# Optimization experiments

Hardware: AMD Instinct MI355X
Metric: run time of the kernel (lower is better)

The kernel has to match this reference:

```python
import jax, jax.numpy as jnp
import numpy as np

N = 100000   # nodes
E = 1600000  # edges
C = 128      # num_features == out_channels
L = 3        # num_layers


def setup_inputs() -> dict:
    key = jax.random.key(0)
    ks = jax.random.split(key, 7)
    x = jax.random.normal(ks[0], (N, C), dtype=jnp.float32)
    edge_index = jax.random.randint(ks[1], (2, E), 0, N, dtype=jnp.int64)
    # GatedGraphConv per-layer linear weights [L, C, C]
    weight = jax.random.normal(ks[2], (L, C, C), dtype=jnp.float32) / np.sqrt(C)
    # shared GRUCell params (torch layout: [3C, C] rows = r, z, n)
    w_ih = jax.random.normal(ks[3], (3 * C, C), dtype=jnp.float32) / np.sqrt(C)
    w_hh = jax.random.normal(ks[4], (3 * C, C), dtype=jnp.float32) / np.sqrt(C)
    b_ih = jax.random.normal(ks[5], (3 * C,), dtype=jnp.float32) * 0.01
    b_hh = jax.random.normal(ks[6], (3 * C,), dtype=jnp.float32) * 0.01
    return {"x": x, "edge_index": edge_index, "weight": weight,
            "w_ih": w_ih, "w_hh": w_hh, "b_ih": b_ih, "b_hh": b_hh}


def _gru_cell(inp, h, w_ih, w_hh, b_ih, b_hh):
    gi = inp @ w_ih.T + b_ih  # [N, 3C]
    gh = h @ w_hh.T + b_hh    # [N, 3C]
    i_r, i_z, i_n = jnp.split(gi, 3, axis=1)
    h_r, h_z, h_n = jnp.split(gh, 3, axis=1)
    r = jax.nn.sigmoid(i_r + h_r)
    z = jax.nn.sigmoid(i_z + h_z)
    n = jnp.tanh(i_n + r * h_n)
    return (1.0 - z) * n + z * h


def reference(x, edge_index, weight, w_ih, w_hh, b_ih, b_hh):
    src, dst = edge_index[0], edge_index[1]
    n_nodes = x.shape[0]
    # mean aggregation denominators (in-degree, 0-degree nodes -> 0 output)
    counts = jax.ops.segment_sum(jnp.ones(src.shape[0], dtype=x.dtype), dst,
                                 num_segments=n_nodes)
    denom = jnp.maximum(counts, 1.0)[:, None]
    h = x
    for i in range(weight.shape[0]):
        m = h @ weight[i]                                   # [N, C]
        agg = jax.ops.segment_sum(m[src], dst, num_segments=n_nodes) / denom
        h = _gru_cell(agg, h, w_ih, w_hh, b_ih, b_hh)
    # x.mean(1).unsqueeze(1) -> [N, 1], then tanh
    return jnp.tanh(jnp.mean(h, axis=1, keepdims=True))
```

## Files before the change

### kernel.cpp

```cpp
#include <hip/hip_runtime.h>
#include <math.h>

#define NN 100000
#define NE 1600000
#define CC 128
#define C3 384
#define SCAN_B 256
#define SCAN_NB ((NN + SCAN_B - 1) / SCAN_B)

typedef __attribute__((ext_vector_type(4))) float f4;
typedef __attribute__((ext_vector_type(8))) short s8;

__device__ __forceinline__ float sigmoidf_(float x) { return 1.0f / (1.0f + __expf(-x)); }
__device__ __forceinline__ float tanhf_(float x) { return 2.0f / (1.0f + __expf(-2.0f * x)) - 1.0f; }

__device__ __forceinline__ short f2bf(float x) {
    unsigned u = __float_as_uint(x);
    unsigned r = (u + 0x7fffu + ((u >> 16) & 1u)) >> 16;
    return (short)r;
}
__device__ __forceinline__ float bf2f(short s) {
    return __uint_as_float(((unsigned)(unsigned short)s) << 16);
}

__device__ __forceinline__ int detect_flag(const int* e32) {
    int allz = 1;
#pragma unroll
    for (int i = 0; i < 32; i++)
        if (e32[2 * i + 1] != 0) allz = 0;
    return allz;
}

__device__ __forceinline__ int edge_val(const void* edges, int f, long long idx) {
    return f ? (int)((const long long*)edges)[idx] : ((const int*)edges)[idx];
}

__global__ void k_count(const void* __restrict__ edges, int* __restrict__ counts) {
    __shared__ int sf;
    if (threadIdx.x == 0) sf = detect_flag((const int*)edges);
    __syncthreads();
    int f = sf;
    int e = blockIdx.x * blockDim.x + threadIdx.x;
    if (e < NE) {
        int d = edge_val(edges, f, (long long)NE + e);
        atomicAdd(&counts[d], 1);
    }
}

__global__ void k_scan1(const int* __restrict__ counts, int* __restrict__ bsum) {
    __shared__ int red[4];
    int t = threadIdx.x;
    int i = blockIdx.x * SCAN_B + t;
    int v = (i < NN) ? counts[i] : 0;
#pragma unroll
    for (int off = 32; off; off >>= 1) v += __shfl_down(v, off);
    if ((t & 63) == 0) red[t >> 6] = v;
    __syncthreads();
    if (t == 0) bsum[blockIdx.x] = red[0] + red[1] + red[2] + red[3];
}

__global__ void k_scan2(const int* __restrict__ bsum, int* __restrict__ boff,
                        int* __restrict__ coarse_cursor) {
    __shared__ int lds[512];
    int t = threadIdx.x;
    int v = (t < SCAN_NB) ? bsum[t] : 0;
    lds[t] = v;
    __syncthreads();
    for (int off = 1; off < 512; off <<= 1) {
        int u = (t >= off) ? lds[t - off] : 0;
        __syncthreads();
        lds[t] += u;
        __syncthreads();
    }
    if (t < SCAN_NB) {
        int ex = lds[t] - v;
        boff[t] = ex;
        coarse_cursor[t] = ex;
    }
}

__global__ void k_scan3(const int* __restrict__ counts, const int* __restrict__ boff,
                        int* __restrict__ rowptr, float* __restrict__ inv_denom) {
    __shared__ int lds[SCAN_B];
    int t = threadIdx.x;
    int i = blockIdx.x * SCAN_B + t;
    int v = (i < NN) ? counts[i] : 0;
    lds[t] = v;
    __syncthreads();
    for (int off = 1; off < SCAN_B; off <<= 1) {
        int u = (t >= off) ? lds[t - off] : 0;
        __syncthreads();
        lds[t] += u;
        __syncthreads();
    }
    if (i < NN) {
        rowptr[i] = boff[blockIdx.x] + lds[t] - v;
        inv_denom[i] = 1.0f / (float)((v > 1) ? v : 1);
    }
    if (i == 0) rowptr[NN] = NE;
}

__global__ __launch_bounds__(1024) void k_part(const void* __restrict__ edges,
                                               int* __restrict__ coarse_cursor,
                                               uint2* __restrict__ tmp) {
    __shared__ int hist[SCAN_NB];
    __shared__ int base[SCAN_NB];
    __shared__ int sf;
    int t = threadIdx.x;
    if (t == 0) sf = detect_flag((const int*)edges);
    long long e0 = (long long)blockIdx.x * 8192;

    for (int c = t; c < SCAN_NB; c += 1024) hist[c] = 0;
    __syncthreads();
    int f = sf;

    int src[8], dst[8];
#pragma unroll
    for (int i = 0; i < 8; i++) {
        long long e = e0 + i * 1024 + t;
        if (e < NE) {
            src[i] = edge_val(edges, f, e);
            dst[i] = edge_val(edges, f, NE + e);
            atomicAdd(&hist[dst[i] >> 8], 1);
        } else {
            dst[i] = -1;
        }
    }
    __syncthreads();
    for (int c = t; c < SCAN_NB; c += 1024) {
        int h = hist[c];
        base[c] = (h > 0) ? atomicAdd(&coarse_cursor[c], h) : 0;
        hist[c] = 0;
    }
    __syncthreads();
#pragma unroll
    for (int i = 0; i < 8; i++) {
        if (dst[i] >= 0) {
            int c = dst[i] >> 8;
            int off = atomicAdd(&hist[c], 1);
            tmp[base[c] + off] = make_uint2((unsigned)src[i], (unsigned)dst[i]);
        }
    }
}

__global__ void k_fine(const uint2* __restrict__ tmp, const int* __restrict__ rowptr,
                       int* __restrict__ csr_src) {
    __shared__ int cur[256];
    int c = blockIdx.x;
    int t = threadIdx.x;
    int d = c * 256 + t;
    cur[t] = (d <= NN) ? rowptr[d < NN ? d : NN] : NE;
    __syncthreads();
    int start = rowptr[c * 256];
    int endd = (c * 256 + 256 <= NN) ? rowptr[c * 256 + 256] : NE;
    for (int p = start + t; p < endd; p += 256) {
        uint2 pr = tmp[p];
        int slot = atomicAdd(&cur[pr.y & 255], 1);
        csr_src[slot] = (int)pr.x;
    }
}

__global__ void k_prep(const float* __restrict__ weight, const float* __restrict__ w_ih,
                       const float* __restrict__ w_hh, const float* __restrict__ b_ih,
                       const float* __restrict__ b_hh,
                       short* __restrict__ B1hi, short* __restrict__ B1lo,
                       short* __restrict__ B2hi, short* __restrict__ B2lo,
                       float* __restrict__ bvec) {
    const int P1 = 3 * C3 * CC;
    int gid = blockIdx.x * blockDim.x + threadIdx.x;
    if (gid < P1) {
        int i = gid / (C3 * CC);
        int rem = gid % (C3 * CC);
        int j = rem / CC;
        int k = rem % CC;
        const float* Wr = weight + i * CC * CC + k * CC;
        const float* ir = w_ih + j * CC;
        float v = 0.f;
#pragma unroll 4
        for (int c = 0; c < CC; c++) v += Wr[c] * ir[c];
        short hi = f2bf(v);
        short lo = f2bf(v - bf2f(hi));
        if (j < 256) {
            int idx = i * 65536 + j * 256 + k;
            B1hi[idx] = hi; B1lo[idx] = lo;
        } else {
            int idx = i * 32768 + (j - 256) * 128 + k;
            B2hi[idx] = hi; B2lo[idx] = lo;
        }
    } else if (gid < 2 * P1) {
        int g = gid - P1;
        int i = g / (C3 * CC);
        int rem = g % (C3 * CC);
        int j = rem / CC;
        int k = rem % CC;
        float v = w_hh[j * CC + k];
        short hi = f2bf(v);
        short lo = f2bf(v - bf2f(hi));
        if (j < 256) {
            int idx = i * 65536 + j * 256 + 128 + k;
            B1hi[idx] = hi; B1lo[idx] = lo;
        } else {
            int idx = i * 32768 + (j - 256 + 128) * 128 + k;
            B2hi[idx] = hi; B2lo[idx] = lo;
        }
    } else if (gid < 2 * P1 + 512) {
        int j = gid - 2 * P1;
        float v;
        if (j < 256) v = b_ih[j] + b_hh[j];
        else if (j < 384) v = b_ih[j];
        else v = b_hh[j - 128];
        bvec[j] = v;
    }
}

__global__ void k_cvt(const float* __restrict__ x, unsigned short* __restrict__ hhi,
                      unsigned short* __restrict__ hlo) {
    long long g = ((long long)blockIdx.x * 256 + threadIdx.x) * 8;
    float4 v0 = *(const float4*)(x + g);
    float4 v1 = *(const float4*)(x + g + 4);
    float f[8] = {v0.x, v0.y, v0.z, v0.w, v1.x, v1.y, v1.z, v1.w};
    s8 oh, ol;
#pragma unroll
    for (int q = 0; q < 8; q++) {
        short hi = f2bf(f[q]);
        oh[q] = hi;
        ol[q] = f2bf(f[q] - bf2f(hi));
    }
    *(s8*)(hhi + g) = oh;
    *(s8*)(hlo + g) = ol;
}

__global__ __launch_bounds__(512, 4) void k_fused(
    const unsigned short* __restrict__ hhi_i, const unsigned short* __restrict__ hlo_i,
    unsigned short* __restrict__ hhi_o, unsigned short* __restrict__ hlo_o,
    const int* __restrict__ rowptr, const int* __restrict__ csr_src,
    const float* __restrict__ inv_denom,
    const short* __restrict__ B1hi, const short* __restrict__ B1lo,
    const short* __restrict__ B2hi, const short* __restrict__ B2lo,
    const float* __restrict__ bvec) {
    __shared__ short Ahi[16384];
    __shared__ short Alo[16384];
    int t = threadIdx.x;
    long long nb = (long long)blockIdx.x * 64;
    int wv = t >> 6;
    int L = t & 63;

#pragma unroll
    for (int i = 0; i < 2; i++) {
        int ci = t + 512 * i;
        int rr = ci >> 4;
        int c = ci & 15;
        int c4 = 16 + c;
        long long row = nb + rr;
        if (row >= NN) row = NN - 1;
        int off = (c4 >> 2) * 2048 + (rr >> 4) * 512 + (rr & 15) * 32 + (c4 & 3) * 8;
        long long gsrc = row * CC + c * 8;
        *(s8*)&Ahi[off] = *(const s8*)(hhi_i + gsrc);
        *(s8*)&Alo[off] = *(const s8*)(hlo_i + gsrc);
    }

    {
        int q = L >> 4;
        int l16 = L & 15;
#pragma unroll
        for (int pass = 0; pass < 2; pass++) {
            int rr = wv * 8 + pass * 4 + q;
            long long rowc = nb + rr;
            if (rowc >= NN) rowc = NN - 1;
            int lo = rowptr[rowc], hi = rowptr[rowc + 1];
            float acc0[8] = {0, 0, 0, 0, 0, 0, 0, 0};
            float acc1[8] = {0, 0, 0, 0, 0, 0, 0, 0};
            int e = lo;
            for (; e + 1 < hi; e += 2) {
                int s0 = csr_src[e];
                int s1 = csr_src[e + 1];
                s8 v0 = ((const s8*)(hhi_i + (long long)s0 * CC))[l16];
                s8 v1 = ((const s8*)(hhi_i + (long long)s1 * CC))[l16];
#pragma unroll
                for (int k = 0; k < 8; k++) {
                    acc0[k] += bf2f(v0[k]);
                    acc1[k] += bf2f(v1[k]);
                }
            }
            if (e < hi) {
                int s0 = csr_src[e];
                s8 v0 = ((const s8*)(hhi_i + (long long)s0 * CC))[l16];
#pragma unroll
                for (int k = 0; k < 8; k++) acc0[k] += bf2f(v0[k]);
            }
            float inv = inv_denom[rowc];
            s8 vh, vl;
#pragma unroll
            for (int k = 0; k < 8; k++) {
                float f = (acc0[k] + acc1[k]) * inv;
                short hi16 = f2bf(f);
                vh[k] = hi16;
                vl[k] = f2bf(f - bf2f(hi16));
            }
            int off = (l16 >> 2) * 2048 + (rr >> 4) * 512 + (rr & 15) * 32 + (l16 & 3) * 8;
            *(s8*)&Ahi[off] = vh;
            *(s8*)&Alo[off] = vl;
        }
    }
    __syncthreads();

    int lm = L & 15;
    int lq = L >> 4;
    int j = wv * 16 + lm;

    f4 aR[4], aZ[4], aN[4], aH[4];
    {
        float bR = bvec[j], bZ = bvec[128 + j], bN = bvec[256 + j], bH = bvec[384 + j];
#pragma unroll
        for (int ch = 0; ch < 4; ch++) {
            aR[ch] = (f4){bR, bR, bR, bR};
            aZ[ch] = (f4){bZ, bZ, bZ, bZ};
            aN[ch] = (f4){bN, bN, bN, bN};
            aH[ch] = (f4){bH, bH, bH, bH};
        }
    }

#pragma unroll
    for (int ks = 0; ks < 8; ks++) {
        int o1 = ks * 32 + lq * 8;
        s8 bRh = *(const s8*)(B1hi + j * 256 + o1);
        s8 bRl = *(const s8*)(B1lo + j * 256 + o1);
        s8 bZh = *(const s8*)(B1hi + (128 + j) * 256 + o1);
        s8 bZl = *(const s8*)(B1lo + (128 + j) * 256 + o1);
        int rowG = (ks < 4) ? j : (128 + j);
        int o2 = (ks & 3) * 32 + lq * 8;
        s8 bGh = *(const s8*)(B2hi + rowG * 128 + o2);
        s8 bGl = *(const s8*)(B2lo + rowG * 128 + o2);
#pragma unroll
        for (int ch = 0; ch < 4; ch++) {
            int aoff = ks * 2048 + ch * 512 + lm * 32 + lq * 8;
            s8 ah = *(const s8*)&Ahi[aoff];
            s8 al = *(const s8*)&Alo[aoff];
            aR[ch] = __builtin_amdgcn_mfma_f32_16x16x32_bf16(ah, bRh, aR[ch], 0, 0, 0);
            aR[ch] = __builtin_amdgcn_mfma_f32_16x16x32_bf16(al, bRh, aR[ch], 0, 0, 0);
            aR[ch] = __builtin_amdgcn_mfma_f32_16x16x32_bf16(ah, bRl, aR[ch], 0, 0, 0);
            aZ[ch] = __builtin_amdgcn_mfma_f32_16x16x32_bf16(ah, bZh, aZ[ch], 0, 0, 0);
            aZ[ch] = __builtin_amdgcn_mfma_f32_16x16x32_bf16(al, bZh, aZ[ch], 0, 0, 0);
            aZ[ch] = __builtin_amdgcn_mfma_f32_16x16x32_bf16(ah, bZl, aZ[ch], 0, 0, 0);
            if (ks < 4) {
                aN[ch] = __builtin_amdgcn_mfma_f32_16x16x32_bf16(ah, bGh, aN[ch], 0, 0, 0);
                aN[ch] = __builtin_amdgcn_mfma_f32_16x16x32_bf16(al, bGh, aN[ch], 0, 0, 0);
                aN[ch] = __builtin_amdgcn_mfma_f32_16x16x32_bf16(ah, bGl, aN[ch], 0, 0, 0);
            } else {
                aH[ch] = __builtin_amdgcn_mfma_f32_16x16x32_bf16(ah, bGh, aH[ch], 0, 0, 0);
                aH[ch] = __builtin_amdgcn_mfma_f32_16x16x32_bf16(al, bGh, aH[ch], 0, 0, 0);
                aH[ch] = __builtin_amdgcn_mfma_f32_16x16x32_bf16(ah, bGl, aH[ch], 0, 0, 0);
            }
        }
    }

    {
        int c4 = 16 + (j >> 3);
        int obase = (c4 >> 2) * 2048 + (c4 & 3) * 8 + (j & 7);
#pragma unroll
        for (int ch = 0; ch < 4; ch++) {
#pragma unroll
            for (int r = 0; r < 4; r++) {
                int node = ch * 16 + lq * 4 + r;
                int off = obase + ch * 512 + (node & 15) * 32;
                float hp = bf2f(Ahi[off]) + bf2f(Alo[off]);
                float sr = aR[ch][r];
                float sz = aZ[ch][r];
                float in_ = aN[ch][r];
                float hn = aH[ch][r];
                float rg = sigmoidf_(sr);
                float zg = sigmoidf_(sz);
                float nv = tanhf_(in_ + rg * hn);
                float val = (1.f - zg) * nv + zg * hp;
                long long gnode = nb + node;
                if (gnode < NN) {
                    long long gd = gnode * CC + j;
                    short vh = f2bf(val);
                    hhi_o[gd] = (unsigned short)vh;
                    hlo_o[gd] = (unsigned short)f2bf(val - bf2f(vh));
                }
            }
        }
    }
}

__global__ void k_out(const unsigned short* __restrict__ hhi,
                      const unsigned short* __restrict__ hlo, float* __restrict__ out) {
    int wid = (blockIdx.x * blockDim.x + threadIdx.x) >> 6;
    int lane = threadIdx.x & 63;
    if (wid >= NN) return;
    ushort2 vh = ((const ushort2*)(hhi + (long long)wid * CC))[lane];
    ushort2 vl = ((const ushort2*)(hlo + (long long)wid * CC))[lane];
    float s = bf2f((short)vh.x) + bf2f((short)vl.x) + bf2f((short)vh.y) + bf2f((short)vl.y);
    for (int off = 32; off; off >>= 1) s += __shfl_down(s, off);
    if (lane == 0) out[wid] = tanhf_(s * (1.0f / 128.0f));
}

extern "C" void kernel_launch(void* const* d_in, const int* in_sizes, int n_in,
                              void* d_out, int out_size, void* d_ws, size_t ws_size,
                              hipStream_t stream) {
    const float* x = (const float*)d_in[0];
    const void* edges = d_in[1];
    const float* weight = (const float*)d_in[2];
    const float* w_ih = (const float*)d_in[3];
    const float* w_hh = (const float*)d_in[4];
    const float* b_ih = (const float*)d_in[5];
    const float* b_hh = (const float*)d_in[6];
    float* out = (float*)d_out;

    char* ws = (char*)d_ws;
    size_t off = 0;
    auto alloc = [&](size_t bytes) -> char* {
        char* p = ws + off;
        off += (bytes + 255) & ~(size_t)255;
        return p;
    };
    int* counts = (int*)alloc((size_t)NN * 4);
    int* rowptr = (int*)alloc((size_t)(NN + 1) * 4);
    int* csr_src = (int*)alloc((size_t)NE * 4);
    float* inv_den = (float*)alloc((size_t)NN * 4);
    int* bsum = (int*)alloc((size_t)SCAN_NB * 4);
    int* boff = (int*)alloc((size_t)SCAN_NB * 4);
    int* coarse_cursor = (int*)alloc((size_t)SCAN_NB * 4);
    uint2* tmp = (uint2*)alloc((size_t)NE * 8);
    short* B1hi = (short*)alloc((size_t)3 * 65536 * 2);
    short* B1lo = (short*)alloc((size_t)3 * 65536 * 2);
    short* B2hi = (short*)alloc((size_t)3 * 32768 * 2);
    short* B2lo = (short*)alloc((size_t)3 * 32768 * 2);
    float* bvec = (float*)alloc(512 * 4);
    unsigned short* hhi0 = (unsigned short*)alloc((size_t)NN * CC * 2);
    unsigned short* hlo0 = (unsigned short*)alloc((size_t)NN * CC * 2);
    unsigned short* hhi1 = (unsigned short*)alloc((size_t)NN * CC * 2);
    unsigned short* hlo1 = (unsigned short*)alloc((size_t)NN * CC * 2);

    hipMemsetAsync(counts, 0, (size_t)NN * 4, stream);

    k_count<<<(NE + 255) / 256, 256, 0, stream>>>(edges, counts);
    k_scan1<<<SCAN_NB, SCAN_B, 0, stream>>>(counts, bsum);
    k_scan2<<<1, 512, 0, stream>>>(bsum, boff, coarse_cursor);
    k_scan3<<<SCAN_NB, SCAN_B, 0, stream>>>(counts, boff, rowptr, inv_den);
    k_part<<<(NE + 8191) / 8192, 1024, 0, stream>>>(edges, coarse_cursor, tmp);
    k_fine<<<SCAN_NB, 256, 0, stream>>>(tmp, rowptr, csr_src);
    int prep_threads = 2 * 3 * C3 * CC + 512;
    k_prep<<<(prep_threads + 255) / 256, 256, 0, stream>>>(weight, w_ih, w_hh, b_ih, b_hh,
                                                           B1hi, B1lo, B2hi, B2lo, bvec);
    k_cvt<<<(NN * CC) / 2048, 256, 0, stream>>>(x, hhi0, hlo0);

    const int blocks = (NN + 63) / 64;
    unsigned short* hi_in = hhi0;  unsigned short* lo_in = hlo0;
    unsigned short* hi_out = hhi1; unsigned short* lo_out = hlo1;
    for (int i = 0; i < 3; i++) {
        k_fused<<<blocks, 512, 0, stream>>>(hi_in, lo_in, hi_out, lo_out,
                                            rowptr, csr_src, inv_den,
                                            B1hi + (size_t)i * 65536, B1lo + (size_t)i * 65536,
                                            B2hi + (size_t)i * 32768, B2lo + (size_t)i * 32768,
                                            bvec);
        unsigned short* th = hi_in; hi_in = hi_out; hi_out = th;
        unsigned short* tl = lo_in; lo_in = lo_out; lo_out = tl;
    }
    k_out<<<25000, 256, 0, stream>>>(hi_in, lo_in, out);
}
```

Baseline: 745.8 us.

## Drop weight low-part MFMAs, unroll gather by four, fuse output reduction into last layer

Weights are now stored only as a single bf16 high part, so the split-precision GEMM drops the third MFMA per accumulator and the low-part weight loads. The neighbour gather loop is unrolled to four edges per iteration to put more loads in flight. The final layer reduces node means into shared memory with atomics and writes tanh outputs directly, which removes the separate output kernel and the final hidden-state store. The trade-off is lower weight precision, which may loosen accuracy, plus shared-memory atomic contention in the last layer.

```diff
diff --git a/kernel.cpp b/kernel.cpp
--- a/kernel.cpp
+++ b/kernel.cpp
@@ -163,8 +163,7 @@
 __global__ void k_prep(const float* __restrict__ weight, const float* __restrict__ w_ih,
                        const float* __restrict__ w_hh, const float* __restrict__ b_ih,
                        const float* __restrict__ b_hh,
-                       short* __restrict__ B1hi, short* __restrict__ B1lo,
-                       short* __restrict__ B2hi, short* __restrict__ B2lo,
+                       short* __restrict__ B1hi, short* __restrict__ B2hi,
                        float* __restrict__ bvec) {
     const int P1 = 3 * C3 * CC;
     int gid = blockIdx.x * blockDim.x + threadIdx.x;
@@ -179,30 +178,17 @@
 #pragma unroll 4
         for (int c = 0; c < CC; c++) v += Wr[c] * ir[c];
         short hi = f2bf(v);
-        short lo = f2bf(v - bf2f(hi));
-        if (j < 256) {
-            int idx = i * 65536 + j * 256 + k;
-            B1hi[idx] = hi; B1lo[idx] = lo;
-        } else {
-            int idx = i * 32768 + (j - 256) * 128 + k;
-            B2hi[idx] = hi; B2lo[idx] = lo;
-        }
+        if (j < 256) B1hi[i * 65536 + j * 256 + k] = hi;
+        else B2hi[i * 32768 + (j - 256) * 128 + k] = hi;
     } else if (gid < 2 * P1) {
         int g = gid - P1;
         int i = g / (C3 * CC);
         int rem = g % (C3 * CC);
         int j = rem / CC;
         int k = rem % CC;
-        float v = w_hh[j * CC + k];
-        short hi = f2bf(v);
-        short lo = f2bf(v - bf2f(hi));
-        if (j < 256) {
-            int idx = i * 65536 + j * 256 + 128 + k;
-            B1hi[idx] = hi; B1lo[idx] = lo;
-        } else {
-            int idx = i * 32768 + (j - 256 + 128) * 128 + k;
-            B2hi[idx] = hi; B2lo[idx] = lo;
-        }
+        short hi = f2bf(w_hh[j * CC + k]);
+        if (j < 256) B1hi[i * 65536 + j * 256 + 128 + k] = hi;
+        else B2hi[i * 32768 + (j - 256 + 128) * 128 + k] = hi;
     } else if (gid < 2 * P1 + 512) {
         int j = gid - 2 * P1;
         float v;
@@ -235,15 +221,17 @@
     unsigned short* __restrict__ hhi_o, unsigned short* __restrict__ hlo_o,
     const int* __restrict__ rowptr, const int* __restrict__ csr_src,
     const float* __restrict__ inv_denom,
-    const short* __restrict__ B1hi, const short* __restrict__ B1lo,
-    const short* __restrict__ B2hi, const short* __restrict__ B2lo,
-    const float* __restrict__ bvec) {
+    const short* __restrict__ B1hi, const short* __restrict__ B2hi,
+    const float* __restrict__ bvec, float* __restrict__ out) {
     __shared__ short Ahi[16384];
     __shared__ short Alo[16384];
+    __shared__ float osum[64];
     int t = threadIdx.x;
     long long nb = (long long)blockIdx.x * 64;
     int wv = t >> 6;
     int L = t & 63;
+
+    if (out && t < 64) osum[t] = 0.f;
 
 #pragma unroll
     for (int i = 0; i < 2; i++) {
@@ -271,6 +259,21 @@
             float acc0[8] = {0, 0, 0, 0, 0, 0, 0, 0};
             float acc1[8] = {0, 0, 0, 0, 0, 0, 0, 0};
             int e = lo;
+            for (; e + 3 < hi; e += 4) {
+                int s0 = csr_src[e];
+                int s1 = csr_src[e + 1];
+                int s2 = csr_src[e + 2];
+                int s3 = csr_src[e + 3];
+                s8 v0 = ((const s8*)(hhi_i + (long long)s0 * CC))[l16];
+                s8 v1 = ((const s8*)(hhi_i + (long long)s1 * CC))[l16];
+                s8 v2 = ((const s8*)(hhi_i + (long long)s2 * CC))[l16];
+                s8 v3 = ((const s8*)(hhi_i + (long long)s3 * CC))[l16];
+#pragma unroll
+                for (int k = 0; k < 8; k++) {
+                    acc0[k] += bf2f(v0[k]) + bf2f(v2[k]);
+                    acc1[k] += bf2f(v1[k]) + bf2f(v3[k]);
+                }
+            }
             for (; e + 1 < hi; e += 2) {
                 int s0 = csr_src[e];
                 int s1 = csr_src[e + 1];
@@ -324,13 +327,10 @@
     for (int ks = 0; ks < 8; ks++) {
         int o1 = ks * 32 + lq * 8;
         s8 bRh = *(const s8*)(B1hi + j * 256 + o1);
-        s8 bRl = *(const s8*)(B1lo + j * 256 + o1);
         s8 bZh = *(const s8*)(B1hi + (128 + j) * 256 + o1);
-        s8 bZl = *(const s8*)(B1lo + (128 + j) * 256 + o1);
         int rowG = (ks < 4) ? j : (128 + j);
         int o2 = (ks & 3) * 32 + lq * 8;
         s8 bGh = *(const s8*)(B2hi + rowG * 128 + o2);
-        s8 bGl = *(const s8*)(B2lo + rowG * 128 + o2);
 #pragma unroll
         for (int ch = 0; ch < 4; ch++) {
             int aoff = ks * 2048 + ch * 512 + lm * 32 + lq * 8;
@@ -338,18 +338,14 @@
             s8 al = *(const s8*)&Alo[aoff];
             aR[ch] = __builtin_amdgcn_mfma_f32_16x16x32_bf16(ah, bRh, aR[ch], 0, 0, 0);
             aR[ch] = __builtin_amdgcn_mfma_f32_16x16x32_bf16(al, bRh, aR[ch], 0, 0, 0);
-            aR[ch] = __builtin_amdgcn_mfma_f32_16x16x32_bf16(ah, bRl, aR[ch], 0, 0, 0);
             aZ[ch] = __builtin_amdgcn_mfma_f32_16x16x32_bf16(ah, bZh, aZ[ch], 0, 0, 0);
             aZ[ch] = __builtin_amdgcn_mfma_f32_16x16x32_bf16(al, bZh, aZ[ch], 0, 0, 0);
-            aZ[ch] = __builtin_amdgcn_mfma_f32_16x16x32_bf16(ah, bZl, aZ[ch], 0, 0, 0);
             if (ks < 4) {
                 aN[ch] = __builtin_amdgcn_mfma_f32_16x16x32_bf16(ah, bGh, aN[ch], 0, 0, 0);
                 aN[ch] = __builtin_amdgcn_mfma_f32_16x16x32_bf16(al, bGh, aN[ch], 0, 0, 0);
-                aN[ch] = __builtin_amdgcn_mfma_f32_16x16x32_bf16(ah, bGl, aN[ch], 0, 0, 0);
             } else {
                 aH[ch] = __builtin_amdgcn_mfma_f32_16x16x32_bf16(ah, bGh, aH[ch], 0, 0, 0);
                 aH[ch] = __builtin_amdgcn_mfma_f32_16x16x32_bf16(al, bGh, aH[ch], 0, 0, 0);
-                aH[ch] = __builtin_amdgcn_mfma_f32_16x16x32_bf16(ah, bGl, aH[ch], 0, 0, 0);
             }
         }
     }
@@ -364,16 +360,14 @@
                 int node = ch * 16 + lq * 4 + r;
                 int off = obase + ch * 512 + (node & 15) * 32;
                 float hp = bf2f(Ahi[off]) + bf2f(Alo[off]);
-                float sr = aR[ch][r];
-                float sz = aZ[ch][r];
-                float in_ = aN[ch][r];
-                float hn = aH[ch][r];
-                float rg = sigmoidf_(sr);
-                float zg = sigmoidf_(sz);
-                float nv = tanhf_(in_ + rg * hn);
+                float rg = sigmoidf_(aR[ch][r]);
+                float zg = sigmoidf_(aZ[ch][r]);
+                float nv = tanhf_(aN[ch][r] + rg * aH[ch][r]);
                 float val = (1.f - zg) * nv + zg * hp;
                 long long gnode = nb + node;
-                if (gnode < NN) {
+                if (out) {
+                    atomicAdd(&osum[node], val);
+                } else if (gnode < NN) {
                     long long gd = gnode * CC + j;
                     short vh = f2bf(val);
                     hhi_o[gd] = (unsigned short)vh;
@@ -382,18 +376,11 @@
             }
         }
     }
-}
-
-__global__ void k_out(const unsigned short* __restrict__ hhi,
-                      const unsigned short* __restrict__ hlo, float* __restrict__ out) {
-    int wid = (blockIdx.x * blockDim.x + threadIdx.x) >> 6;
-    int lane = threadIdx.x & 63;
-    if (wid >= NN) return;
-    ushort2 vh = ((const ushort2*)(hhi + (long long)wid * CC))[lane];
-    ushort2 vl = ((const ushort2*)(hlo + (long long)wid * CC))[lane];
-    float s = bf2f((short)vh.x) + bf2f((short)vl.x) + bf2f((short)vh.y) + bf2f((short)vl.y);
-    for (int off = 32; off; off >>= 1) s += __shfl_down(s, off);
-    if (lane == 0) out[wid] = tanhf_(s * (1.0f / 128.0f));
+    if (out) {
+        __syncthreads();
+        if (t < 64 && nb + t < NN)
+            out[nb + t] = tanhf_(osum[t] * (1.0f / 128.0f));
+    }
 }
 
 extern "C" void kernel_launch(void* const* d_in, const int* in_sizes, int n_in,
@@ -424,9 +411,7 @@
     int* coarse_cursor = (int*)alloc((size_t)SCAN_NB * 4);
     uint2* tmp = (uint2*)alloc((size_t)NE * 8);
     short* B1hi = (short*)alloc((size_t)3 * 65536 * 2);
-    short* B1lo = (short*)alloc((size_t)3 * 65536 * 2);
     short* B2hi = (short*)alloc((size_t)3 * 32768 * 2);
-    short* B2lo = (short*)alloc((size_t)3 * 32768 * 2);
     float* bvec = (float*)alloc(512 * 4);
     unsigned short* hhi0 = (unsigned short*)alloc((size_t)NN * CC * 2);
     unsigned short* hlo0 = (unsigned short*)alloc((size_t)NN * CC * 2);
@@ -443,20 +428,20 @@
     k_fine<<<SCAN_NB, 256, 0, stream>>>(tmp, rowptr, csr_src);
     int prep_threads = 2 * 3 * C3 * CC + 512;
     k_prep<<<(prep_threads + 255) / 256, 256, 0, stream>>>(weight, w_ih, w_hh, b_ih, b_hh,
-                                                           B1hi, B1lo, B2hi, B2lo, bvec);
+                                                           B1hi, B2hi, bvec);
     k_cvt<<<(NN * CC) / 2048, 256, 0, stream>>>(x, hhi0, hlo0);
 
     const int blocks = (NN + 63) / 64;
     unsigned short* hi_in = hhi0;  unsigned short* lo_in = hlo0;
     unsigned short* hi_out = hhi1; unsigned short* lo_out = hlo1;
     for (int i = 0; i < 3; i++) {
+        float* outp = (i == 2) ? out : nullptr;
         k_fused<<<blocks, 512, 0, stream>>>(hi_in, lo_in, hi_out, lo_out,
                                             rowptr, csr_src, inv_den,
-                                            B1hi + (size_t)i * 65536, B1lo + (size_t)i * 65536,
-                                            B2hi + (size_t)i * 32768, B2lo + (size_t)i * 32768,
-                                            bvec);
+                                            B1hi + (size_t)i * 65536,
+                                            B2hi + (size_t)i * 32768,
+                                            bvec, outp);
         unsigned short* th = hi_in; hi_in = hi_out; hi_out = th;
         unsigned short* tl = lo_in; lo_in = lo_out; lo_out = tl;
     }
-    k_out<<<25000, 256, 0, stream>>>(hi_in, lo_in, out);
-}
+}
```

After: 639.0 us. 1.17x faster.
